# Optimization experiments

Measured on AMD Instinct MI355X. Metric: run time of the kernel, lower is better.

The kernel has to match this reference:

```python
import jax, jax.numpy as jnp
import numpy as np

D_MODEL = 512
NUM_HEADS = 8
DEPTH = D_MODEL // NUM_HEADS
NEG_INF = -1e9


def setup_inputs() -> dict:
    key = jax.random.key(0)
    ks = jax.random.split(key, 12)
    B, S = 4, 2048
    scale = 1.0 / np.sqrt(D_MODEL)
    inp = {
        "q": jax.random.normal(ks[0], (B, S, D_MODEL), jnp.float32),
        "k": jax.random.normal(ks[1], (B, S, D_MODEL), jnp.float32),
        "v": jax.random.normal(ks[2], (B, S, D_MODEL), jnp.float32),
        "mask": jnp.zeros((1, 1, S, S), jnp.float32),
        # Dense layer params (keras Dense = x @ W + b)
        "wq": jax.random.normal(ks[3], (D_MODEL, D_MODEL), jnp.float32) * scale,
        "bq": jnp.zeros((D_MODEL,), jnp.float32),
        "wk": jax.random.normal(ks[4], (D_MODEL, D_MODEL), jnp.float32) * scale,
        "bk": jnp.zeros((D_MODEL,), jnp.float32),
        "wv": jax.random.normal(ks[5], (D_MODEL, D_MODEL), jnp.float32) * scale,
        "bv": jnp.zeros((D_MODEL,), jnp.float32),
        "wo": jax.random.normal(ks[6], (D_MODEL, D_MODEL), jnp.float32) * scale,
        "bo": jnp.zeros((D_MODEL,), jnp.float32),
    }
    return inp


def _split_heads(x):
    # [B, S, D] -> [B, H, S, depth]
    B, S, _ = x.shape
    return x.reshape(B, S, NUM_HEADS, DEPTH).transpose(0, 2, 1, 3)


def reference(q, k, v, mask, wq, bq, wk, bk, wv, bv, wo, bo):
    B, S, _ = q.shape
    qh = _split_heads(q @ wq + bq)  # [B,H,S,depth]
    kh = _split_heads(k @ wk + bk)
    vh = _split_heads(v @ wv + bv)
    logits = jnp.einsum("bhqd,bhkd->bhqk", qh, kh) / jnp.sqrt(
        jnp.asarray(DEPTH, qh.dtype)
    )
    logits = logits + mask * NEG_INF
    attn = jax.nn.softmax(logits, axis=-1)
    out = jnp.einsum("bhqk,bhkd->bhqd", attn, vh)  # [B,H,S,depth]
    out = out.transpose(0, 2, 1, 3).reshape(B, S, D_MODEL)
    return out @ wo + bo
```

## Files before the change

kernel.cpp:

```cpp
#include <hip/hip_runtime.h>
#include <hip/hip_bf16.h>

#define S_LEN 2048
#define DM    512
#define NH    8
#define DH    64

typedef float  f4   __attribute__((ext_vector_type(4)));
typedef float  f16v __attribute__((ext_vector_type(16)));
typedef short  s8v  __attribute__((ext_vector_type(8)));
typedef __bf16 b8v  __attribute__((ext_vector_type(8)));
union F8 { s8v s; b8v b; };
union U4 { unsigned u[4]; s8v s; b8v b; };

typedef __attribute__((address_space(1))) const void gas_t;
typedef __attribute__((address_space(3))) void       las_t;

__device__ __forceinline__ void gl16(const void* g, void* l) {
  __builtin_amdgcn_global_load_lds((gas_t*)g, (las_t*)l, 16, 0, 0);
}

__device__ __forceinline__ ushort f2bf(float x) {
  unsigned u = __float_as_uint(x);
  u += 0x7FFFu + ((u >> 16) & 1u);
  return (ushort)(u >> 16);
}
__device__ __forceinline__ unsigned pk2(float a, float b) {
  union { __hip_bfloat162 h; unsigned u; } cv;
  cv.h = __float22bfloat162_rn(make_float2(a, b));
  return cv.u;
}
__device__ __forceinline__ unsigned pkt(float a, float b) {
  return __builtin_amdgcn_perm(__float_as_uint(b), __float_as_uint(a),
                               0x07060302u);
}
__device__ __forceinline__ float ex2(float x) {
#if __has_builtin(__builtin_amdgcn_exp2f)
  return __builtin_amdgcn_exp2f(x);
#else
  return exp2f(x);
#endif
}

__device__ __forceinline__ void plswap(unsigned a, unsigned b,
                                       unsigned& lo, unsigned& hi2) {
#if __has_builtin(__builtin_amdgcn_permlane32_swap)
  auto r = __builtin_amdgcn_permlane32_swap((int)a, (int)b, false, false);
  lo  = (unsigned)r[0];
  hi2 = (unsigned)r[1];
#else
  const bool ish = (threadIdx.x & 32) != 0;
  const unsigned sa = (unsigned)__shfl_xor((int)a, 32);
  const unsigned sb = (unsigned)__shfl_xor((int)b, 32);
  lo  = ish ? sb : a;
  hi2 = ish ? b  : sa;
#endif
}

__global__ void prep(const float* __restrict__ q, const float* __restrict__ k,
                     const float* __restrict__ v, const float* __restrict__ mask,
                     const float* __restrict__ w0, const float* __restrict__ w1,
                     const float* __restrict__ w2, const float* __restrict__ w3,
                     ushort* __restrict__ oq, ushort* __restrict__ ok,
                     ushort* __restrict__ ov, ushort* __restrict__ o0,
                     ushort* __restrict__ o1, ushort* __restrict__ o2,
                     ushort* __restrict__ o3, int* __restrict__ flag) {
  const int z = blockIdx.y;
  if (z == 5) {
    const int bx = blockIdx.x;
    if (bx >= 1024) return;
    const int w = bx >> 8;
    const float* src = (w == 0) ? w0 : (w == 1) ? w1 : (w == 2) ? w2 : w3;
    ushort* dst = (w == 0) ? o0 : (w == 1) ? o1 : (w == 2) ? o2 : o3;
    __shared__ float tile[32][33];
    const int tx = threadIdx.x & 31, ty = threadIdx.x >> 5;
    const int k0 = (bx & 15) * 32, n0 = ((bx >> 4) & 15) * 32;
#pragma unroll
    for (int i = 0; i < 4; ++i)
      tile[ty + i * 8][tx] = src[(size_t)(k0 + ty + i * 8) * DM + n0 + tx];
    __syncthreads();
#pragma unroll
    for (int i = 0; i < 4; ++i)
      dst[(size_t)(n0 + ty + i * 8) * DM + k0 + tx] = f2bf(tile[tx][ty + i * 8]);
    return;
  }
  if (z >= 3) {
    const size_t i = (((size_t)(z - 3) * 2048 + blockIdx.x) * 256 + threadIdx.x) * 4;
    const float4 m4 = *(const float4*)(mask + i);
    const bool nz = (m4.x != 0.f) | (m4.y != 0.f) | (m4.z != 0.f) | (m4.w != 0.f);
    if (nz) atomicOr(flag, 1);
    return;
  }
  const float* s = (z == 0) ? q : (z == 1) ? k : v;
  ushort* d = (z == 0) ? oq : (z == 1) ? ok : ov;
  const size_t i = ((size_t)blockIdx.x * 256 + threadIdx.x) * 8;
  const float4 a = *(const float4*)(s + i);
  const float4 b = *(const float4*)(s + i + 4);
  s8v r;
  r[0] = (short)f2bf(a.x); r[1] = (short)f2bf(a.y);
  r[2] = (short)f2bf(a.z); r[3] = (short)f2bf(a.w);
  r[4] = (short)f2bf(b.x); r[5] = (short)f2bf(b.y);
  r[6] = (short)f2bf(b.z); r[7] = (short)f2bf(b.w);
  *(s8v*)(d + i) = r;
}

__device__ __forceinline__ void gemm_core(
    const ushort* __restrict__ A, const ushort* __restrict__ Bt,
    const float* __restrict__ bias, void* __restrict__ out, int mode,
    ushort* As, ushort* Bs, int tm, int tn) {
  const int tid  = threadIdx.x;
  const int lane = tid & 63, wave = tid >> 6;
  const int ql = lane & 15, lg = lane >> 4;
  const int wr = wave >> 1, wc = wave & 1;

  const int srow  = wave * 32 + (lane >> 2);
  const int sbyte = (lane & 3) * 16;

  const char* gA = (const char*)(A  + (size_t)(tm * 128 + srow) * 512) + sbyte;
  const char* gB = (const char*)(Bt + (size_t)(tn * 128 + srow) * 512) + sbyte;

  auto stage = [&](int kt, int buf) {
    const size_t gofs = (size_t)kt * 64;
    char* lA = (char*)As + buf * 8192 + wave * 2048;
    char* lB = (char*)Bs + buf * 8192 + wave * 2048;
    gl16(gA + gofs, lA);
    gl16(gA + gofs + 16 * 512 * 2, lA + 1024);
    gl16(gB + gofs, lB);
    gl16(gB + gofs + 16 * 512 * 2, lB + 1024);
  };

  f4 acc[4][4] = {};

  stage(0, 0);
  __syncthreads();

  int cur = 0;
  for (int kt = 0; kt < 16; ++kt) {
    if (kt + 1 < 16) stage(kt + 1, cur ^ 1);
    const ushort* Ab = As + cur * 4096;
    const ushort* Bb = Bs + cur * 4096;
    F8 af[4], bf[4];
#pragma unroll
    for (int i = 0; i < 4; ++i) {
      af[i].s = *(const s8v*)(Ab + (wr * 64 + i * 16 + ql) * 32 + lg * 8);
      bf[i].s = *(const s8v*)(Bb + (wc * 64 + i * 16 + ql) * 32 + lg * 8);
    }
#pragma unroll
    for (int i = 0; i < 4; ++i)
#pragma unroll
      for (int j = 0; j < 4; ++j)
        acc[i][j] = __builtin_amdgcn_mfma_f32_16x16x32_bf16(af[i].b, bf[j].b,
                                                            acc[i][j], 0, 0, 0);
    __syncthreads();
    cur ^= 1;
  }

#pragma unroll
  for (int i = 0; i < 4; ++i) {
#pragma unroll
    for (int j = 0; j < 4; ++j) {
      const int n = tn * 128 + wc * 64 + j * 16 + ql;
      const float bz = bias[n];
#pragma unroll
      for (int r = 0; r < 4; ++r) {
        const int m = tm * 128 + wr * 64 + i * 16 + lg * 4 + r;
        const float val = acc[i][j][r] + bz;
        if (mode == 2) {
          ((float*)out)[(size_t)m * DM + n] = val;
        } else {
          const int b = m >> 11, s = m & 2047, h = n >> 6, d = n & 63;
          if (mode == 0)
            ((ushort*)out)[((size_t)(b * NH + h) * S_LEN + s) * DH + d] = f2bf(val);
          else
            ((ushort*)out)[((size_t)(b * NH + h) * DH + d) * S_LEN + s] = f2bf(val);
        }
      }
    }
  }
}

__global__ __launch_bounds__(256) void gemm_qkv(
    const ushort* __restrict__ Xq, const ushort* __restrict__ Xk,
    const ushort* __restrict__ Xv, const ushort* __restrict__ Wtq,
    const ushort* __restrict__ Wtk, const ushort* __restrict__ Wtv,
    const float* __restrict__ bq, const float* __restrict__ bk,
    const float* __restrict__ bv, ushort* __restrict__ Qh,
    ushort* __restrict__ Kh, ushort* __restrict__ Vt) {
  __shared__ ushort As[2 * 128 * 32], Bs[2 * 128 * 32];
  const int b = blockIdx.x;
  const int xcd = b & 7, i = b >> 3;
  const int z = i >> 5, j = i & 31;
  const int tm = xcd * 8 + (j >> 2), tn = j & 3;
  const ushort* A  = (z == 0) ? Xq : (z == 1) ? Xk : Xv;
  const ushort* Bp = (z == 0) ? Wtq : (z == 1) ? Wtk : Wtv;
  const float* bias = (z == 0) ? bq : (z == 1) ? bk : bv;
  void* out = (z == 0) ? (void*)Qh : (z == 1) ? (void*)Kh : (void*)Vt;
  gemm_core(A, Bp, bias, out, (z == 2) ? 1 : 0, As, Bs, tm, tn);
}

__global__ __launch_bounds__(256) void gemm_o2(
    const ushort* __restrict__ Obf, const ushort* __restrict__ Wto,
    const float* __restrict__ bo, float* __restrict__ out) {
  __shared__ ushort As[2 * 128 * 32];
  __shared__ ushort Bs[2 * 64 * 32];
  const int bidx = blockIdx.x;
  const int xcd = bidx & 7, ii = bidx >> 3;
  const int tm = xcd * 8 + (ii >> 3), tn = ii & 7;
  const int tid  = threadIdx.x;
  const int lane = tid & 63, wave = tid >> 6;
  const int ql = lane & 15, lg = lane >> 4;
  const int wr = wave >> 1, wc = wave & 1;

  const int rowA0 = tid >> 2,         offA0 = (tid & 3) * 16;
  const int rowA1 = (256 + tid) >> 2, offA1 = ((256 + tid) & 3) * 16;
  const int rowB  = tid >> 2,         offB  = (tid & 3) * 16;
  const char* gA0 = (const char*)(Obf + (size_t)(tm * 128 + rowA0) * 512) + offA0;
  const char* gA1 = (const char*)(Obf + (size_t)(tm * 128 + rowA1) * 512) + offA1;
  const char* gB  = (const char*)(Wto + (size_t)(tn * 64 + rowB) * 512) + offB;

  auto stage = [&](int kt, int buf) {
    const size_t gofs = (size_t)kt * 64;
    char* lA0 = (char*)As + buf * 8192 + wave * 1024;
    char* lA1 = (char*)As + buf * 8192 + 4096 + wave * 1024;
    char* lB  = (char*)Bs + buf * 4096 + wave * 1024;
    gl16(gA0 + gofs, lA0);
    gl16(gA1 + gofs, lA1);
    gl16(gB + gofs, lB);
  };

  f4 acc[4][2] = {};

  stage(0, 0);
  __syncthreads();

  int cur = 0;
  for (int kt = 0; kt < 16; ++kt) {
    if (kt + 1 < 16) stage(kt + 1, cur ^ 1);
    const ushort* Ab = As + cur * 4096;
    const ushort* Bb = Bs + cur * 2048;
    F8 af[4], bf[2];
#pragma unroll
    for (int i = 0; i < 4; ++i)
      af[i].s = *(const s8v*)(Ab + (wr * 64 + i * 16 + ql) * 32 + lg * 8);
#pragma unroll
    for (int j = 0; j < 2; ++j)
      bf[j].s = *(const s8v*)(Bb + (wc * 32 + j * 16 + ql) * 32 + lg * 8);
#pragma unroll
    for (int i = 0; i < 4; ++i)
#pragma unroll
      for (int j = 0; j < 2; ++j)
        acc[i][j] = __builtin_amdgcn_mfma_f32_16x16x32_bf16(af[i].b, bf[j].b,
                                                            acc[i][j], 0, 0, 0);
    __syncthreads();
    cur ^= 1;
  }

#pragma unroll
  for (int i = 0; i < 4; ++i)
#pragma unroll
    for (int j = 0; j < 2; ++j) {
      const int n = tn * 64 + wc * 32 + j * 16 + ql;
      const float bz = bo[n];
#pragma unroll
      for (int r = 0; r < 4; ++r) {
        const int m = tm * 128 + wr * 64 + i * 16 + lg * 4 + r;
        out[(size_t)m * DM + n] = acc[i][j][r] + bz;
      }
    }
}

__global__ __launch_bounds__(256, 2) void attn(
    const ushort* __restrict__ Qh, const ushort* __restrict__ Kh,
    const ushort* __restrict__ Vt, const float* __restrict__ mask,
    const int* __restrict__ flagp, ushort* __restrict__ Obf) {
  __shared__ ushort Ks[2][4096];
  __shared__ ushort Vs[2][4096];

  const float K2 = 0.18033688011f;
  const float C2 = 17.3095245361f;

  const int bid = (blockIdx.x & 7) * 64 + (blockIdx.x >> 3);
  const int bh = bid >> 4, qb = bid & 15;
  const int tid = threadIdx.x, lane = tid & 63, wave = tid >> 6;
  const int cl = lane & 31, hi = lane >> 5;
  const int q = qb * 128 + wave * 32 + cl;
  const bool um = (*flagp) != 0;
  const char* KbC = (const char*)(Kh + (size_t)bh * S_LEN * DH);
  const char* VbC = (const char*)(Vt + (size_t)bh * DH * S_LEN);
  const unsigned swz = (unsigned)((cl & 7) << 4);

  int kofs[2], vofs[2];
#pragma unroll
  for (int c = 0; c < 2; ++c) {
    const int ui  = wave * 128 + c * 64 + lane;
    const int row = ui >> 3, u = ui & 7;
    const int xu  = u ^ (row & 7);
    kofs[c] = row * 128  + (xu << 4);
    vofs[c] = row * 4096 + (xu << 4);
  }

  F8 qf[4];
#pragma unroll
  for (int c = 0; c < 4; ++c)
    qf[c].s = *(const s8v*)(Qh + ((size_t)bh * S_LEN + q) * DH + hi * 8 + 16 * c);

  F8 ones;
#pragma unroll
  for (int i = 0; i < 8; ++i) ones.s[i] = (short)0x3F80;

  f16v oacc0 = {}, oacc1 = {}, sacc = {};

  {
    char* kl = (char*)&Ks[0][0] + wave * 2048;
    char* vl = (char*)&Vs[0][0] + wave * 2048;
    gl16(KbC + kofs[0], kl);
    gl16(KbC + kofs[1], kl + 1024);
    gl16(VbC + vofs[0], vl);
    gl16(VbC + vofs[1], vl + 1024);
  }
  __syncthreads();

  int cur = 0;
  for (int kt = 0; kt < 32; ++kt) {
    if (kt + 1 < 32) {
      const char* kg = KbC + (size_t)(kt + 1) * 8192;
      const char* vg = VbC + (size_t)(kt + 1) * 128;
      char* kl = (char*)&Ks[cur ^ 1][0] + wave * 2048;
      char* vl = (char*)&Vs[cur ^ 1][0] + wave * 2048;
      gl16(kg + kofs[0], kl);
      gl16(kg + kofs[1], kl + 1024);
      gl16(vg + vofs[0], vl);
      gl16(vg + vofs[1], vl + 1024);
    }

    const int kv0 = kt * 64;
    const char* KtB = (const char*)&Ks[cur][0];
    const char* VtB = (const char*)&Vs[cur][0];

    const char* kr0 = KtB + (size_t)cl * 128;
    const char* kr1 = KtB + (size_t)(32 + cl) * 128;
    f16v s0 = {}, s1 = {};
    __builtin_amdgcn_s_setprio(1);
#pragma unroll
    for (int c = 0; c < 4; ++c) {
      const unsigned off = ((unsigned)(hi * 16 + 32 * c)) ^ swz;
      F8 ka0, ka1;
      ka0.s = *(const s8v*)(kr0 + off);
      ka1.s = *(const s8v*)(kr1 + off);
      s0 = __builtin_amdgcn_mfma_f32_32x32x16_bf16(ka0.b, qf[c].b, s0, 0, 0, 0);
      s1 = __builtin_amdgcn_mfma_f32_32x32x16_bf16(ka1.b, qf[c].b, s1, 0, 0, 0);
    }
    __builtin_amdgcn_s_setprio(0);

    if (um) {
#pragma unroll
      for (int r = 0; r < 16; ++r) {
        const int kvr = kv0 + (r & 3) + 8 * (r >> 2) + 4 * hi;
        s0[r] += mask[(size_t)q * S_LEN + kvr] * (-8e9f);
        s1[r] += mask[(size_t)q * S_LEN + kvr + 32] * (-8e9f);
      }
    }

#pragma unroll
    for (int r = 0; r < 16; ++r) {
      s0[r] = ex2(fmaf(s0[r], K2, -C2));
      s1[r] = ex2(fmaf(s1[r], K2, -C2));
    }

    unsigned P0[4][2], P1[4][2];
#pragma unroll
    for (int u = 0; u < 4; ++u)
#pragma unroll
      for (int e = 0; e < 2; ++e) {
        P0[u][e] = pkt(s0[4 * u + 2 * e], s0[4 * u + 2 * e + 1]);
        P1[u][e] = pkt(s1[4 * u + 2 * e], s1[4 * u + 2 * e + 1]);
      }
    U4 pf[4];
#pragma unroll
    for (int half = 0; half < 2; ++half)
#pragma unroll
      for (int e = 0; e < 2; ++e) {
        unsigned lo, h2;
        plswap(P0[2 * half][e], P0[2 * half + 1][e], lo, h2);
        pf[half].u[e] = lo; pf[half].u[2 + e] = h2;
        plswap(P1[2 * half][e], P1[2 * half + 1][e], lo, h2);
        pf[2 + half].u[e] = lo; pf[2 + half].u[2 + e] = h2;
      }

    const char* vr0 = VtB + (size_t)cl * 128;
    const char* vr1 = VtB + (size_t)(32 + cl) * 128;
    __builtin_amdgcn_s_setprio(1);
#pragma unroll
    for (int c = 0; c < 4; ++c) {
      const unsigned off = ((unsigned)(hi * 16 + 32 * c)) ^ swz;
      F8 va0, va1;
      va0.s = *(const s8v*)(vr0 + off);
      va1.s = *(const s8v*)(vr1 + off);
      oacc0 = __builtin_amdgcn_mfma_f32_32x32x16_bf16(va0.b, pf[c].b, oacc0, 0, 0, 0);
      oacc1 = __builtin_amdgcn_mfma_f32_32x32x16_bf16(va1.b, pf[c].b, oacc1, 0, 0, 0);
      sacc  = __builtin_amdgcn_mfma_f32_32x32x16_bf16(ones.b, pf[c].b, sacc, 0, 0, 0);
    }
    __builtin_amdgcn_s_setprio(0);

    __syncthreads();
    cur ^= 1;
  }

  const float inv = 1.f / sacc[0];
  const int b = bh >> 3, h = bh & 7;
  ushort* op = Obf + ((size_t)(b * S_LEN + q)) * DM + h * DH;
#pragma unroll
  for (int u = 0; u < 4; ++u) {
    const int d0 = 8 * u + 4 * hi;
    *(uint2*)(op + d0) =
        make_uint2(pk2(oacc0[4 * u] * inv, oacc0[4 * u + 1] * inv),
                   pk2(oacc0[4 * u + 2] * inv, oacc0[4 * u + 3] * inv));
    *(uint2*)(op + 32 + d0) =
        make_uint2(pk2(oacc1[4 * u] * inv, oacc1[4 * u + 1] * inv),
                   pk2(oacc1[4 * u + 2] * inv, oacc1[4 * u + 3] * inv));
  }
}

extern "C" void kernel_launch(void* const* d_in, const int* in_sizes, int n_in,
                              void* d_out, int out_size, void* d_ws, size_t ws_size,
                              hipStream_t stream) {
  (void)in_sizes; (void)n_in; (void)out_size; (void)ws_size;
  const float* q    = (const float*)d_in[0];
  const float* k    = (const float*)d_in[1];
  const float* v    = (const float*)d_in[2];
  const float* mask = (const float*)d_in[3];
  const float* wq   = (const float*)d_in[4];
  const float* bq   = (const float*)d_in[5];
  const float* wk   = (const float*)d_in[6];
  const float* bk   = (const float*)d_in[7];
  const float* wv   = (const float*)d_in[8];
  const float* bv   = (const float*)d_in[9];
  const float* wo   = (const float*)d_in[10];
  const float* bo   = (const float*)d_in[11];

  char* ws = (char*)d_ws;
  const size_t SZX = (size_t)8192 * 512 * 2;
  ushort* Xq  = (ushort*)(ws + 0 * SZX);
  ushort* Xk  = (ushort*)(ws + 1 * SZX);
  ushort* Xv  = (ushort*)(ws + 2 * SZX);
  ushort* Qh  = (ushort*)(ws + 3 * SZX);
  ushort* Kh  = (ushort*)(ws + 4 * SZX);
  ushort* Vt  = (ushort*)(ws + 5 * SZX);
  ushort* Obf = Xq;
  const size_t SZW = (size_t)512 * 512 * 2;
  ushort* Wtq = (ushort*)(ws + 6 * SZX + 0 * SZW);
  ushort* Wtk = (ushort*)(ws + 6 * SZX + 1 * SZW);
  ushort* Wtv = (ushort*)(ws + 6 * SZX + 2 * SZW);
  ushort* Wto = (ushort*)(ws + 6 * SZX + 3 * SZW);
  int* flag   = (int*)(ws + 6 * SZX + 4 * SZW);

  hipMemsetAsync(flag, 0, 4, stream);
  prep<<<dim3(2048, 6), 256, 0, stream>>>(q, k, v, mask, wq, wk, wv, wo,
                                          Xq, Xk, Xv, Wtq, Wtk, Wtv, Wto, flag);
  gemm_qkv<<<768, 256, 0, stream>>>(Xq, Xk, Xv, Wtq, Wtk, Wtv,
                                    bq, bk, bv, Qh, Kh, Vt);
  attn<<<512, 256, 0, stream>>>(Qh, Kh, Vt, mask, flag, Obf);
  gemm_o2<<<512, 256, 0, stream>>>(Obf, Wto, bo, (float*)d_out);
}
```

Measured before the change: 114.2 us.

## Fuse fp32-to-bf16 activation conversion into the QKV projection GEMM

Removes the separate prep pass that converted q, k and v from fp32 to bf16 in a workspace. The QKV GEMM now loads fp32 activations into registers, packs them to bf16 and writes them to LDS itself, overlapping the next tile's load with the current MFMAs. Only the weight staging keeps the async global-to-LDS path. This saves one full write and read of the bf16 activation copies, but doubles the A-operand global bytes inside the GEMM and adds register pressure and VALU conversion work.

```diff
diff --git a/kernel.cpp b/kernel.cpp
--- a/kernel.cpp
+++ b/kernel.cpp
@@ -57,16 +57,14 @@
 #endif
 }
 
-__global__ void prep(const float* __restrict__ q, const float* __restrict__ k,
-                     const float* __restrict__ v, const float* __restrict__ mask,
+__global__ void prep(const float* __restrict__ mask,
                      const float* __restrict__ w0, const float* __restrict__ w1,
                      const float* __restrict__ w2, const float* __restrict__ w3,
-                     ushort* __restrict__ oq, ushort* __restrict__ ok,
-                     ushort* __restrict__ ov, ushort* __restrict__ o0,
-                     ushort* __restrict__ o1, ushort* __restrict__ o2,
-                     ushort* __restrict__ o3, int* __restrict__ flag) {
+                     ushort* __restrict__ o0, ushort* __restrict__ o1,
+                     ushort* __restrict__ o2, ushort* __restrict__ o3,
+                     int* __restrict__ flag) {
   const int z = blockIdx.y;
-  if (z == 5) {
+  if (z == 2) {
     const int bx = blockIdx.x;
     if (bx >= 1024) return;
     const int w = bx >> 8;
@@ -84,118 +82,111 @@
       dst[(size_t)(n0 + ty + i * 8) * DM + k0 + tx] = f2bf(tile[tx][ty + i * 8]);
     return;
   }
-  if (z >= 3) {
-    const size_t i = (((size_t)(z - 3) * 2048 + blockIdx.x) * 256 + threadIdx.x) * 4;
-    const float4 m4 = *(const float4*)(mask + i);
-    const bool nz = (m4.x != 0.f) | (m4.y != 0.f) | (m4.z != 0.f) | (m4.w != 0.f);
-    if (nz) atomicOr(flag, 1);
-    return;
-  }
-  const float* s = (z == 0) ? q : (z == 1) ? k : v;
-  ushort* d = (z == 0) ? oq : (z == 1) ? ok : ov;
-  const size_t i = ((size_t)blockIdx.x * 256 + threadIdx.x) * 8;
-  const float4 a = *(const float4*)(s + i);
-  const float4 b = *(const float4*)(s + i + 4);
-  s8v r;
-  r[0] = (short)f2bf(a.x); r[1] = (short)f2bf(a.y);
-  r[2] = (short)f2bf(a.z); r[3] = (short)f2bf(a.w);
-  r[4] = (short)f2bf(b.x); r[5] = (short)f2bf(b.y);
-  r[6] = (short)f2bf(b.z); r[7] = (short)f2bf(b.w);
-  *(s8v*)(d + i) = r;
-}
-
-__device__ __forceinline__ void gemm_core(
-    const ushort* __restrict__ A, const ushort* __restrict__ Bt,
-    const float* __restrict__ bias, void* __restrict__ out, int mode,
-    ushort* As, ushort* Bs, int tm, int tn) {
-  const int tid  = threadIdx.x;
-  const int lane = tid & 63, wave = tid >> 6;
-  const int ql = lane & 15, lg = lane >> 4;
-  const int wr = wave >> 1, wc = wave & 1;
-
-  const int srow  = wave * 32 + (lane >> 2);
-  const int sbyte = (lane & 3) * 16;
-
-  const char* gA = (const char*)(A  + (size_t)(tm * 128 + srow) * 512) + sbyte;
-  const char* gB = (const char*)(Bt + (size_t)(tn * 128 + srow) * 512) + sbyte;
-
-  auto stage = [&](int kt, int buf) {
-    const size_t gofs = (size_t)kt * 64;
-    char* lA = (char*)As + buf * 8192 + wave * 2048;
-    char* lB = (char*)Bs + buf * 8192 + wave * 2048;
-    gl16(gA + gofs, lA);
-    gl16(gA + gofs + 16 * 512 * 2, lA + 1024);
-    gl16(gB + gofs, lB);
-    gl16(gB + gofs + 16 * 512 * 2, lB + 1024);
-  };
-
-  f4 acc[4][4] = {};
-
-  stage(0, 0);
-  __syncthreads();
-
-  int cur = 0;
-  for (int kt = 0; kt < 16; ++kt) {
-    if (kt + 1 < 16) stage(kt + 1, cur ^ 1);
-    const ushort* Ab = As + cur * 4096;
-    const ushort* Bb = Bs + cur * 4096;
-    F8 af[4], bf[4];
-#pragma unroll
-    for (int i = 0; i < 4; ++i) {
-      af[i].s = *(const s8v*)(Ab + (wr * 64 + i * 16 + ql) * 32 + lg * 8);
-      bf[i].s = *(const s8v*)(Bb + (wc * 64 + i * 16 + ql) * 32 + lg * 8);
-    }
-#pragma unroll
-    for (int i = 0; i < 4; ++i)
-#pragma unroll
-      for (int j = 0; j < 4; ++j)
-        acc[i][j] = __builtin_amdgcn_mfma_f32_16x16x32_bf16(af[i].b, bf[j].b,
-                                                            acc[i][j], 0, 0, 0);
-    __syncthreads();
-    cur ^= 1;
-  }
-
-#pragma unroll
-  for (int i = 0; i < 4; ++i) {
-#pragma unroll
-    for (int j = 0; j < 4; ++j) {
-      const int n = tn * 128 + wc * 64 + j * 16 + ql;
-      const float bz = bias[n];
-#pragma unroll
-      for (int r = 0; r < 4; ++r) {
-        const int m = tm * 128 + wr * 64 + i * 16 + lg * 4 + r;
-        const float val = acc[i][j][r] + bz;
-        if (mode == 2) {
-          ((float*)out)[(size_t)m * DM + n] = val;
-        } else {
-          const int b = m >> 11, s = m & 2047, h = n >> 6, d = n & 63;
-          if (mode == 0)
-            ((ushort*)out)[((size_t)(b * NH + h) * S_LEN + s) * DH + d] = f2bf(val);
-          else
-            ((ushort*)out)[((size_t)(b * NH + h) * DH + d) * S_LEN + s] = f2bf(val);
-        }
-      }
-    }
-  }
+  const size_t i = (((size_t)z * 2048 + blockIdx.x) * 256 + threadIdx.x) * 4;
+  const float4 m4 = *(const float4*)(mask + i);
+  const bool nz = (m4.x != 0.f) | (m4.y != 0.f) | (m4.z != 0.f) | (m4.w != 0.f);
+  if (nz) atomicOr(flag, 1);
 }
 
 __global__ __launch_bounds__(256) void gemm_qkv(
-    const ushort* __restrict__ Xq, const ushort* __restrict__ Xk,
-    const ushort* __restrict__ Xv, const ushort* __restrict__ Wtq,
+    const float* __restrict__ Qf, const float* __restrict__ Kf,
+    const float* __restrict__ Vf, const ushort* __restrict__ Wtq,
     const ushort* __restrict__ Wtk, const ushort* __restrict__ Wtv,
     const float* __restrict__ bq, const float* __restrict__ bk,
     const float* __restrict__ bv, ushort* __restrict__ Qh,
     ushort* __restrict__ Kh, ushort* __restrict__ Vt) {
   __shared__ ushort As[2 * 128 * 32], Bs[2 * 128 * 32];
+
   const int b = blockIdx.x;
   const int xcd = b & 7, i = b >> 3;
   const int z = i >> 5, j = i & 31;
   const int tm = xcd * 8 + (j >> 2), tn = j & 3;
-  const ushort* A  = (z == 0) ? Xq : (z == 1) ? Xk : Xv;
-  const ushort* Bp = (z == 0) ? Wtq : (z == 1) ? Wtk : Wtv;
+  const float* A = (z == 0) ? Qf : (z == 1) ? Kf : Vf;
+  const ushort* Bt = (z == 0) ? Wtq : (z == 1) ? Wtk : Wtv;
   const float* bias = (z == 0) ? bq : (z == 1) ? bk : bv;
-  void* out = (z == 0) ? (void*)Qh : (z == 1) ? (void*)Kh : (void*)Vt;
-  gemm_core(A, Bp, bias, out, (z == 2) ? 1 : 0, As, Bs, tm, tn);
+  ushort* out = (z == 0) ? Qh : (z == 1) ? Kh : Vt;
+  const int mode = (z == 2) ? 1 : 0;
+
+  const int tid  = threadIdx.x;
+  const int lane = tid & 63, wave = tid >> 6;
+  const int ql = lane & 15, lg = lane >> 4;
+  const int wr = wave >> 1, wc = wave & 1;
+
+  const int srow = wave * 32 + (lane >> 2);
+  const float* gA0 = A + (size_t)(tm * 128 + srow) * 512 + (lane & 3) * 8;
+  const float* gA1 = gA0 + 16 * 512;
+  const char*  gB  = (const char*)(Bt + (size_t)(tn * 128 + srow) * 512) +
+                     (lane & 3) * 16;
+
+  float4 ar[4];
+  auto loadA = [&](int kt) {
+    const float* p0 = gA0 + kt * 32;
+    const float* p1 = gA1 + kt * 32;
+    ar[0] = *(const float4*)p0; ar[1] = *(const float4*)(p0 + 4);
+    ar[2] = *(const float4*)p1; ar[3] = *(const float4*)(p1 + 4);
+  };
+  auto writeA = [&](int buf) {
+    char* d = (char*)As + buf * 8192 + srow * 64 + (lane & 3) * 16;
+    *(uint4*)d = make_uint4(pk2(ar[0].x, ar[0].y), pk2(ar[0].z, ar[0].w),
+                            pk2(ar[1].x, ar[1].y), pk2(ar[1].z, ar[1].w));
+    *(uint4*)(d + 16 * 64) =
+        make_uint4(pk2(ar[2].x, ar[2].y), pk2(ar[2].z, ar[2].w),
+                   pk2(ar[3].x, ar[3].y), pk2(ar[3].z, ar[3].w));
+  };
+  auto stageB = [&](int kt, int buf) {
+    char* lB = (char*)Bs + buf * 8192 + wave * 2048;
+    const size_t gofs = (size_t)kt * 64;
+    gl16(gB + gofs, lB);
+    gl16(gB + gofs + 16 * 512 * 2, lB + 1024);
+  };
+
+  f4 acc[4][4] = {};
+
+  loadA(0);
+  stageB(0, 0);
+  writeA(0);
+  __syncthreads();
+
+  int cur = 0;
+  for (int kt = 0; kt < 16; ++kt) {
+    if (kt + 1 < 16) { loadA(kt + 1); stageB(kt + 1, cur ^ 1); }
+    const ushort* Ab = As + cur * 4096;
+    const ushort* Bb = Bs + cur * 4096;
+    F8 af[4], bf[4];
+#pragma unroll
+    for (int ii = 0; ii < 4; ++ii) {
+      af[ii].s = *(const s8v*)(Ab + (wr * 64 + ii * 16 + ql) * 32 + lg * 8);
+      bf[ii].s = *(const s8v*)(Bb + (wc * 64 + ii * 16 + ql) * 32 + lg * 8);
+    }
+#pragma unroll
+    for (int ii = 0; ii < 4; ++ii)
+#pragma unroll
+      for (int jj = 0; jj < 4; ++jj)
+        acc[ii][jj] = __builtin_amdgcn_mfma_f32_16x16x32_bf16(
+            af[ii].b, bf[jj].b, acc[ii][jj], 0, 0, 0);
+    if (kt + 1 < 16) writeA(cur ^ 1);
+    __syncthreads();
+    cur ^= 1;
+  }
+
+#pragma unroll
+  for (int ii = 0; ii < 4; ++ii) {
+#pragma unroll
+    for (int jj = 0; jj < 4; ++jj) {
+      const int n = tn * 128 + wc * 64 + jj * 16 + ql;
+      const float bz = bias[n];
+#pragma unroll
+      for (int r = 0; r < 4; ++r) {
+        const int m = tm * 128 + wr * 64 + ii * 16 + lg * 4 + r;
+        const float val = acc[ii][jj][r] + bz;
+        const int bb = m >> 11, s = m & 2047, h = n >> 6, d = n & 63;
+        if (mode == 0)
+          out[((size_t)(bb * NH + h) * S_LEN + s) * DH + d] = f2bf(val);
+        else
+          out[((size_t)(bb * NH + h) * DH + d) * S_LEN + s] = f2bf(val);
+      }
+    }
+  }
 }
 
 __global__ __launch_bounds__(256) void gemm_o2(
@@ -440,13 +431,10 @@
 
   char* ws = (char*)d_ws;
   const size_t SZX = (size_t)8192 * 512 * 2;
-  ushort* Xq  = (ushort*)(ws + 0 * SZX);
-  ushort* Xk  = (ushort*)(ws + 1 * SZX);
-  ushort* Xv  = (ushort*)(ws + 2 * SZX);
+  ushort* Obf = (ushort*)(ws + 0 * SZX);
   ushort* Qh  = (ushort*)(ws + 3 * SZX);
   ushort* Kh  = (ushort*)(ws + 4 * SZX);
   ushort* Vt  = (ushort*)(ws + 5 * SZX);
-  ushort* Obf = Xq;
   const size_t SZW = (size_t)512 * 512 * 2;
   ushort* Wtq = (ushort*)(ws + 6 * SZX + 0 * SZW);
   ushort* Wtk = (ushort*)(ws + 6 * SZX + 1 * SZW);
@@ -455,9 +443,9 @@
   int* flag   = (int*)(ws + 6 * SZX + 4 * SZW);
 
   hipMemsetAsync(flag, 0, 4, stream);
-  prep<<<dim3(2048, 6), 256, 0, stream>>>(q, k, v, mask, wq, wk, wv, wo,
-                                          Xq, Xk, Xv, Wtq, Wtk, Wtv, Wto, flag);
-  gemm_qkv<<<768, 256, 0, stream>>>(Xq, Xk, Xv, Wtq, Wtk, Wtv,
+  prep<<<dim3(2048, 3), 256, 0, stream>>>(mask, wq, wk, wv, wo,
+                                          Wtq, Wtk, Wtv, Wto, flag);
+  gemm_qkv<<<768, 256, 0, stream>>>(q, k, v, Wtq, Wtk, Wtv,
                                     bq, bk, bv, Qh, Kh, Vt);
   attn<<<512, 256, 0, stream>>>(Qh, Kh, Vt, mask, flag, Obf);
   gemm_o2<<<512, 256, 0, stream>>>(Obf, Wto, bo, (float*)d_out);
```

New measurement: 109.1 us. 4.4% less time.
